# Optimization experiments

Measured on AMD Instinct MI355X. Metric: run time of the kernel, lower is better.

## Reference

```python
import jax, jax.numpy as jnp
import numpy as np

B, T, D, H = 2, 2048, 1024, 16
DK = D // H


def setup_inputs() -> dict:
    key = jax.random.key(0)
    ks = jax.random.split(key, 9)
    x = jax.random.normal(ks[0], (B, T, D), dtype=jnp.float32)
    # causal mask, broadcastable to [B, H, T, T]; positions with 0 are masked
    mask = jnp.tril(jnp.ones((T, T), dtype=jnp.int32))[None, None]
    s = 1.0 / np.sqrt(D)
    Wq = jax.random.normal(ks[1], (D, D), dtype=jnp.float32) * s
    Wk = jax.random.normal(ks[2], (D, D), dtype=jnp.float32) * s
    Wv = jax.random.normal(ks[3], (D, D), dtype=jnp.float32) * s
    Wo = jax.random.normal(ks[4], (D, D), dtype=jnp.float32) * s
    bq = jnp.zeros((D,), jnp.float32)
    bk = jnp.zeros((D,), jnp.float32)
    bv = jnp.zeros((D,), jnp.float32)
    bo = jnp.zeros((D,), jnp.float32)
    return {"x": x, "mask": mask, "Wq": Wq, "bq": bq, "Wk": Wk, "bk": bk,
            "Wv": Wv, "bv": bv, "Wo": Wo, "bo": bo}


def _split_heads(t):
    # [B, T, D] -> [B, H, T, DK]
    return t.reshape(B, T, H, DK).transpose(0, 2, 1, 3)


def reference(x, mask, Wq, bq, Wk, bk, Wv, bv, Wo, bo):
    Q = _split_heads(x @ Wq.T + bq)
    K = _split_heads(x @ Wk.T + bk)
    V = _split_heads(x @ Wv.T + bv)
    scores = jnp.einsum('bhqd,bhkd->bhqk', Q, K) / jnp.sqrt(jnp.float32(DK))
    scores = jnp.where(mask == 0, jnp.float32(-1e9), scores)
    attn = jax.nn.softmax(scores, axis=-1)  # dropout p=0 -> identity
    out = jnp.einsum('bhqk,bhkd->bhqd', attn, V)
    out = out.transpose(0, 2, 1, 3).reshape(B, T, D)
    out = out @ Wo.T + bo
    return (out, attn)
```

## Files before the change

### kernel.cpp

```cpp
#include <hip/hip_runtime.h>
#include <hip/hip_bf16.h>
#include <cstdint>


typedef __attribute__((ext_vector_type(8))) short bf16x8;
typedef __attribute__((ext_vector_type(4))) float f32x4;

#define MFMA(a,b,c) __builtin_amdgcn_mfma_f32_16x16x32_bf16((a),(b),(c),0,0,0)

static __device__ __forceinline__ short f2bf(float f) {
  __hip_bfloat16 h = __float2bfloat16(f);
  return (short)__builtin_bit_cast(ushort, h);
}

static __device__ __forceinline__ bf16x8 cvt8(const float* p) {
  float4 v0 = *(const float4*)p;
  float4 v1 = *(const float4*)(p + 4);
  bf16x8 r;
  r[0] = f2bf(v0.x); r[1] = f2bf(v0.y); r[2] = f2bf(v0.z); r[3] = f2bf(v0.w);
  r[4] = f2bf(v1.x); r[5] = f2bf(v1.y); r[6] = f2bf(v1.z); r[7] = f2bf(v1.w);
  return r;
}

static __device__ __forceinline__ size_t wbf_off(int J, int k) {
  return (size_t)((J >> 9) * 2048 + 1536 + (J & 511)) * 4096 + k;
}

__global__ __launch_bounds__(256)
void cvt_xw(const float* __restrict__ x,
            const float* __restrict__ Wq, const float* __restrict__ Wk,
            const float* __restrict__ Wv,
            ushort* __restrict__ xbf, ushort* __restrict__ attnU)
{
  if (blockIdx.x < 2048) {
    const size_t i = ((size_t)blockIdx.x * 256 + threadIdx.x) * 8;
    *(bf16x8*)&xbf[i] = cvt8(x + i);
  } else {
    const size_t e = ((size_t)(blockIdx.x - 2048) * 256 + threadIdx.x) * 8;
    const int J = (int)(e >> 10);
    const int k = (int)(e & 1023);
    const int widx = J >> 10, j = J & 1023;
    const float* W = (widx == 0) ? Wq : ((widx == 1) ? Wk : Wv);
    const bf16x8 v = cvt8(W + (size_t)j * 1024 + k);
    *(bf16x8*)&attnU[wbf_off(J, k)] = v;
  }
}

__global__ __launch_bounds__(256)
void qkv_zeros(const ushort* __restrict__ Xbf, const ushort* __restrict__ WbfU,
               const float* __restrict__ bq, const float* __restrict__ bk,
               const float* __restrict__ bv,
               ushort* __restrict__ Qw, ushort* __restrict__ Kw, ushort* __restrict__ Vt,
               float* __restrict__ attn)
{
  __shared__ __align__(16) ushort As[128 * 32];
  __shared__ __align__(16) ushort Bs[128 * 32];
  const int tid  = threadIdx.x;
  const int lane = tid & 63;
  const int wid  = tid >> 6;

  if (blockIdx.x >= 768) {
    const int zi = blockIdx.x - 768;
    const int qtile = zi % 31;
    const int bh = zi / 31;
    const int zstart = (qtile + 1) * 64;
    const int zlen = 2048 - zstart;
    float* base = attn + ((size_t)bh * 2048 + qtile * 64) * 2048;
    const f32x4 z = (f32x4){0.f, 0.f, 0.f, 0.f};
#pragma unroll
    for (int rr = 0; rr < 16; ++rr) {
      float* rowp = base + (size_t)(wid * 16 + rr) * 2048 + zstart;
      for (int c = lane * 4; c < zlen; c += 256)
        __builtin_nontemporal_store(z, (f32x4*)(rowp + c));
    }
    return;
  }

  const int wr = wid >> 1, wc = wid & 1;
  const int g = lane >> 4, c16 = lane & 15;
  const int i0 = (blockIdx.x & 31) * 128;
  const int j0 = (blockIdx.x >> 5) * 128;

  const int widx = j0 >> 10;
  const int jj0  = j0 & 1023;
  const float* bias = (widx == 0) ? bq : ((widx == 1) ? bk : bv);

  const int arow = tid >> 2;
  const int acol = (tid & 3) * 8;
  const ushort* a0p = Xbf + (size_t)(i0 + arow) * 1024 + acol;
  const ushort* a1p = a0p + (size_t)64 * 1024;
  const int J0 = widx * 1024 + jj0 + arow;
  const ushort* b0p = WbfU + wbf_off(J0, acol);
  const ushort* b1p = WbfU + wbf_off(J0 + 64, acol);

  f32x4 acc[4][4];
#pragma unroll
  for (int mi = 0; mi < 4; ++mi)
#pragma unroll
    for (int ni = 0; ni < 4; ++ni) acc[mi][ni] = (f32x4){0.f, 0.f, 0.f, 0.f};

  for (int k0 = 0; k0 < 1024; k0 += 32) {
    const bf16x8 va0 = *(const bf16x8*)(a0p + k0);
    const bf16x8 va1 = *(const bf16x8*)(a1p + k0);
    const bf16x8 vb0 = *(const bf16x8*)(b0p + k0);
    const bf16x8 vb1 = *(const bf16x8*)(b1p + k0);
    __syncthreads();
    *(bf16x8*)&As[tid * 8]        = va0;
    *(bf16x8*)&As[2048 + tid * 8] = va1;
    *(bf16x8*)&Bs[tid * 8]        = vb0;
    *(bf16x8*)&Bs[2048 + tid * 8] = vb1;
    __syncthreads();
    bf16x8 af[4], bfv[4];
#pragma unroll
    for (int mi = 0; mi < 4; ++mi)
      af[mi] = *(const bf16x8*)&As[(wr * 64 + mi * 16 + c16) * 32 + g * 8];
#pragma unroll
    for (int ni = 0; ni < 4; ++ni)
      bfv[ni] = *(const bf16x8*)&Bs[(wc * 64 + ni * 16 + c16) * 32 + g * 8];
#pragma unroll
    for (int mi = 0; mi < 4; ++mi)
#pragma unroll
      for (int ni = 0; ni < 4; ++ni)
        acc[mi][ni] = MFMA(af[mi], bfv[ni], acc[mi][ni]);
  }

  float bv4[4];
#pragma unroll
  for (int ni = 0; ni < 4; ++ni) bv4[ni] = bias[jj0 + wc * 64 + ni * 16 + c16];

  if (widx < 2) {
    ushort* OP = (widx == 0) ? Qw : Kw;
#pragma unroll
    for (int mi = 0; mi < 4; ++mi) {
      const int ib = i0 + wr * 64 + mi * 16 + g * 4;
      const int b = ib >> 11, t = ib & 2047;
#pragma unroll
      for (int ni = 0; ni < 4; ++ni) {
        const int jj = jj0 + wc * 64 + ni * 16 + c16;
        const int h = jj >> 6, dk = jj & 63;
        const size_t base = ((size_t)(b * 16 + h) * 2048 + t) * 64 + dk;
#pragma unroll
        for (int r = 0; r < 4; ++r)
          OP[base + (size_t)r * 64] = (ushort)f2bf(acc[mi][ni][r] + bv4[ni]);
      }
    }
  } else {
#pragma unroll
    for (int mi = 0; mi < 4; ++mi) {
      const int ib = i0 + wr * 64 + mi * 16 + g * 4;
      const int b = ib >> 11, t = ib & 2047;
#pragma unroll
      for (int ni = 0; ni < 4; ++ni) {
        const int jj = jj0 + wc * 64 + ni * 16 + c16;
        ushort4 pk;
        pk.x = (ushort)f2bf(acc[mi][ni][0] + bv4[ni]);
        pk.y = (ushort)f2bf(acc[mi][ni][1] + bv4[ni]);
        pk.z = (ushort)f2bf(acc[mi][ni][2] + bv4[ni]);
        pk.w = (ushort)f2bf(acc[mi][ni][3] + bv4[ni]);
        *(ushort4*)&Vt[((size_t)b * 1024 + jj) * 2048 + t] = pk;
      }
    }
  }
}

__global__ __launch_bounds__(512)
void attn_stats(const ushort* __restrict__ Qw, const ushort* __restrict__ Kw,
                const ushort* __restrict__ Vt, ushort* __restrict__ ctx,
                float* __restrict__ Linv)
{
  __shared__ __align__(16) ushort Ks[2][64][68];
  __shared__ __align__(16) ushort Vs[2][64][68];
  __shared__ __align__(16) ushort Plds[8][16][68];
  const int tid = threadIdx.x, lane = tid & 63, wid = tid >> 6;
  const int g = lane >> 4, c16 = lane & 15;
  const int pr = blockIdx.x;
  const int bh = blockIdx.y;
  const int b = bh >> 4, h = bh & 15;

  const ushort* kbase = Kw + (size_t)bh * (2048 * 64);
  const ushort* vbase = Vt + ((size_t)b * 1024 + h * 64) * 2048;

  const int sr = tid >> 3;
  const int sc = (tid & 7) * 8;
  const ushort* kst = kbase + (size_t)sr * 64 + sc;
  const ushort* vst = vbase + (size_t)sr * 2048 + sc;

  int cur = 0;

#pragma unroll
  for (int part = 0; part < 2; ++part) {
    const int jt = part ? (15 - pr) : pr;
    const int qt = jt * 128 + wid * 16;
    const int q = qt + c16;
    const int nch = 2 * jt + 2;

    const ushort* qp = Qw + ((size_t)bh * 2048 + q) * 64 + g * 8;
    const bf16x8 qf0 = *(const bf16x8*)qp;
    const bf16x8 qf1 = *(const bf16x8*)(qp + 32);

    f32x4 o[4];
#pragma unroll
    for (int dt = 0; dt < 4; ++dt) o[dt] = (f32x4){0.f, 0.f, 0.f, 0.f};
    float lsum = 0.f;

    {
      const bf16x8 k0 = *(const bf16x8*)kst;
      const bf16x8 v0 = *(const bf16x8*)vst;
      __syncthreads();
      *(bf16x8*)&Ks[cur][sr][sc] = k0;
      *(bf16x8*)&Vs[cur][sr][sc] = v0;
    }

    for (int c = 0; c < nch; ++c) {
      bf16x8 kn, vn;
      const bool pf = (c + 1 < nch);
      if (pf) {
        const int kt1 = (c + 1) * 64;
        kn = *(const bf16x8*)(kst + (size_t)kt1 * 64);
        vn = *(const bf16x8*)(vst + kt1);
      }
      __syncthreads();

      const int kt = c * 64;
      f32x4 sv[4];
#pragma unroll
      for (int s = 0; s < 4; ++s) {
        const bf16x8 kf0 = *(const bf16x8*)&Ks[cur][s * 16 + c16][g * 8];
        const bf16x8 kf1 = *(const bf16x8*)&Ks[cur][s * 16 + c16][32 + g * 8];
        f32x4 t0 = (f32x4){0.f, 0.f, 0.f, 0.f};
        t0 = MFMA(kf0, qf0, t0);
        t0 = MFMA(kf1, qf1, t0);
        sv[s] = t0;
      }

#pragma unroll
      for (int s = 0; s < 4; ++s) {
        short pk[4];
#pragma unroll
        for (int r = 0; r < 4; ++r) {
          const int k = kt + s * 16 + g * 4 + r;
          const float p = (k > q) ? 0.f : __expf(sv[s][r] * 0.125f - 20.f);
          lsum += p;
          pk[r] = f2bf(p);
        }
        *(short4*)&Plds[wid][c16][s * 16 + g * 4] = *(short4*)pk;
      }

      {
        const bf16x8 pa0 = *(const bf16x8*)&Plds[wid][c16][g * 8];
#pragma unroll
        for (int dt = 0; dt < 4; ++dt) {
          const bf16x8 vf = *(const bf16x8*)&Vs[cur][dt * 16 + c16][g * 8];
          o[dt] = MFMA(pa0, vf, o[dt]);
        }
        const bf16x8 pa1 = *(const bf16x8*)&Plds[wid][c16][32 + g * 8];
#pragma unroll
        for (int dt = 0; dt < 4; ++dt) {
          const bf16x8 vf = *(const bf16x8*)&Vs[cur][dt * 16 + c16][32 + g * 8];
          o[dt] = MFMA(pa1, vf, o[dt]);
        }
      }

      if (pf) {
        *(bf16x8*)&Ks[cur ^ 1][sr][sc] = kn;
        *(bf16x8*)&Vs[cur ^ 1][sr][sc] = vn;
        cur ^= 1;
      }
    }

    lsum += __shfl_xor(lsum, 16);
    lsum += __shfl_xor(lsum, 32);
    const float linv = 1.f / lsum;
    if (g == 0) Linv[(size_t)bh * 2048 + q] = linv;

#pragma unroll
    for (int r = 0; r < 4; ++r) {
      const float lr = __shfl(linv, g * 4 + r);
#pragma unroll
      for (int dt = 0; dt < 4; ++dt)
        ctx[((size_t)(b * 2048 + qt + g * 4 + r)) * 1024 + h * 64 + dt * 16 + c16] =
            (ushort)f2bf(o[dt][r] * lr);
    }
  }
}

__global__ __launch_bounds__(256)
void out_tiles(const ushort* __restrict__ Qw, const ushort* __restrict__ Kw,
               const float* __restrict__ Linv, float* __restrict__ attn,
               const ushort* __restrict__ ctx, const float* __restrict__ Wo,
               const float* __restrict__ bo, float* __restrict__ out)
{
  __shared__ __align__(16) ushort As[128 * 32];
  __shared__ __align__(16) ushort Bs[128 * 32];
  __shared__ __align__(16) float Pst[4][16][72];
  const int tid = threadIdx.x, lane = tid & 63, wid = tid >> 6;
  const int g = lane >> 4, c16 = lane & 15;

  if (blockIdx.x >= 256) {
    const int ti = blockIdx.x - 256;
    const int bx = ti % 132;
    const int bh = ti / 132;
    const int n = bx * 4 + wid;
    int qtile = (int)((sqrtf(8.f * n + 1.f) - 1.f) * 0.5f);
    while ((qtile + 1) * (qtile + 2) / 2 <= n) ++qtile;
    while (qtile * (qtile + 1) / 2 > n) --qtile;
    const int ktile = n - qtile * (qtile + 1) / 2;
    const int qt0 = qtile * 64, kt0 = ktile * 64;
    float* abase = attn + ((size_t)bh * 2048) * 2048;

    const ushort* qbase = Qw + ((size_t)bh * 2048 + qt0) * 64;
    const ushort* kbase = Kw + ((size_t)bh * 2048 + kt0) * 64;
    bf16x8 qf0[4], qf1[4], kf0[4], kf1[4];
    float lv[4];
#pragma unroll
    for (int sq = 0; sq < 4; ++sq) {
      const ushort* qp = qbase + (size_t)(sq * 16 + c16) * 64 + g * 8;
      qf0[sq] = *(const bf16x8*)qp;
      qf1[sq] = *(const bf16x8*)(qp + 32);
      lv[sq] = Linv[(size_t)bh * 2048 + qt0 + sq * 16 + c16];
    }
#pragma unroll
    for (int sk = 0; sk < 4; ++sk) {
      const ushort* kp = kbase + (size_t)(sk * 16 + c16) * 64 + g * 8;
      kf0[sk] = *(const bf16x8*)kp;
      kf1[sk] = *(const bf16x8*)(kp + 32);
    }

    const bool diag = (ktile == qtile);
    const int rrow = lane >> 4;
    const int rcol = (lane & 15) * 4;

#pragma unroll
    for (int sq = 0; sq < 4; ++sq) {
      const int qq = qt0 + sq * 16 + c16;
#pragma unroll
      for (int sk = 0; sk < 4; ++sk) {
        f32x4 t = (f32x4){0.f, 0.f, 0.f, 0.f};
        t = MFMA(kf0[sk], qf0[sq], t);
        t = MFMA(kf1[sk], qf1[sq], t);
        f32x4 st;
        if (diag) {
#pragma unroll
          for (int r = 0; r < 4; ++r) {
            const int kk = kt0 + sk * 16 + g * 4 + r;
            st[r] = (kk > qq) ? 0.f : __expf(t[r] * 0.125f - 20.f) * lv[sq];
          }
        } else {
#pragma unroll
          for (int r = 0; r < 4; ++r)
            st[r] = __expf(t[r] * 0.125f - 20.f) * lv[sq];
        }
        *(f32x4*)&Pst[wid][c16][sk * 16 + g * 4] = st;
      }
#pragma unroll
      for (int rr = 0; rr < 4; ++rr) {
        const int row = rr * 4 + rrow;
        const f32x4 v = *(const f32x4*)&Pst[wid][row][rcol];
        __builtin_nontemporal_store(v,
            (f32x4*)(abase + (size_t)(qt0 + sq * 16 + row) * 2048 + kt0 + rcol));
      }
    }
    return;
  }

  const int j = blockIdx.x;
  const int wr = wid >> 1, wc = wid & 1;
  const int i0 = (j & 31) * 128;
  const int j0 = (j >> 5) * 128;

  const int arow = tid >> 2;
  const int acol = (tid & 3) * 8;
  const ushort* a0p = ctx + (size_t)(i0 + arow) * 1024 + acol;
  const ushort* a1p = a0p + (size_t)64 * 1024;
  const float*  b0p = Wo + (size_t)(j0 + arow) * 1024 + acol;
  const float*  b1p = b0p + (size_t)64 * 1024;

  f32x4 acc[4][4];
#pragma unroll
  for (int mi = 0; mi < 4; ++mi)
#pragma unroll
    for (int ni = 0; ni < 4; ++ni) acc[mi][ni] = (f32x4){0.f, 0.f, 0.f, 0.f};

  for (int k0 = 0; k0 < 1024; k0 += 32) {
    const bf16x8 va0 = *(const bf16x8*)(a0p + k0);
    const bf16x8 va1 = *(const bf16x8*)(a1p + k0);
    const bf16x8 vb0 = cvt8(b0p + k0);
    const bf16x8 vb1 = cvt8(b1p + k0);
    __syncthreads();
    *(bf16x8*)&As[tid * 8]        = va0;
    *(bf16x8*)&As[2048 + tid * 8] = va1;
    *(bf16x8*)&Bs[tid * 8]        = vb0;
    *(bf16x8*)&Bs[2048 + tid * 8] = vb1;
    __syncthreads();
    bf16x8 af[4], bfv[4];
#pragma unroll
    for (int mi = 0; mi < 4; ++mi)
      af[mi] = *(const bf16x8*)&As[(wr * 64 + mi * 16 + c16) * 32 + g * 8];
#pragma unroll
    for (int ni = 0; ni < 4; ++ni)
      bfv[ni] = *(const bf16x8*)&Bs[(wc * 64 + ni * 16 + c16) * 32 + g * 8];
#pragma unroll
    for (int mi = 0; mi < 4; ++mi)
#pragma unroll
      for (int ni = 0; ni < 4; ++ni)
        acc[mi][ni] = MFMA(af[mi], bfv[ni], acc[mi][ni]);
  }

  float bv4[4];
#pragma unroll
  for (int ni = 0; ni < 4; ++ni) bv4[ni] = bo[j0 + wc * 64 + ni * 16 + c16];

#pragma unroll
  for (int mi = 0; mi < 4; ++mi) {
    const int ib = i0 + wr * 64 + mi * 16 + g * 4;
#pragma unroll
    for (int ni = 0; ni < 4; ++ni) {
      const int jj = j0 + wc * 64 + ni * 16 + c16;
#pragma unroll
      for (int r = 0; r < 4; ++r)
        out[(size_t)(ib + r) * 1024 + jj] = acc[mi][ni][r] + bv4[ni];
    }
  }
}

extern "C" void kernel_launch(void* const* d_in, const int* in_sizes, int n_in,
                              void* d_out, int out_size, void* d_ws, size_t ws_size,
                              hipStream_t stream)
{
  const float* x  = (const float*)d_in[0];
  const float* Wq = (const float*)d_in[2];
  const float* bq = (const float*)d_in[3];
  const float* Wk = (const float*)d_in[4];
  const float* bk = (const float*)d_in[5];
  const float* Wv = (const float*)d_in[6];
  const float* bv = (const float*)d_in[7];
  const float* Wo = (const float*)d_in[8];
  const float* bo = (const float*)d_in[9];

  if (ws_size < (size_t)33816576) return;

  float* out  = (float*)d_out;
  float* attn = out + (size_t)4194304;
  ushort* attnU = (ushort*)attn;

  ushort* ws   = (ushort*)d_ws;
  ushort* Qw   = ws;
  ushort* Kw   = Qw + (size_t)4194304;
  ushort* Vtw  = Kw + (size_t)4194304;
  ushort* ctx  = Vtw + (size_t)4194304;
  float*  Linv = (float*)(ctx + (size_t)4194304);

  cvt_xw<<<dim3(3584), 256, 0, stream>>>(x, Wq, Wk, Wv, ctx, attnU);
  qkv_zeros<<<dim3(1760), 256, 0, stream>>>(ctx, attnU, bq, bk, bv,
                                            Qw, Kw, Vtw, attn);
  attn_stats<<<dim3(8, 32), 512, 0, stream>>>(Qw, Kw, Vtw, ctx, Linv);
  out_tiles<<<dim3(4480), 256, 0, stream>>>(Qw, Kw, Linv, attn, ctx, Wo, bo, out);
}
```

Baseline: 220.2 us.

## Write attention probabilities as 64x256 strips staged through shared memory

The attention-probability writer now has each block cover a 64-row by 256-column strip. The four waves compute adjacent 64x64 tiles into a shared staging buffer, and the block then stores full 1 KB row segments, replacing per-wave 256-byte row pieces. Zero-filling of the masked region in the earlier kernel now starts at 256-column strip boundaries, so the strip kernel writes the zeros inside partially masked strips. This trades larger shared memory use and a block barrier for fewer, more contiguous global stores, and it reorders the strip schedule so the largest strips run first.

```diff
diff --git a/kernel.cpp b/kernel.cpp
--- a/kernel.cpp
+++ b/kernel.cpp
@@ -61,9 +61,9 @@
 
   if (blockIdx.x >= 768) {
     const int zi = blockIdx.x - 768;
-    const int qtile = zi % 31;
-    const int bh = zi / 31;
-    const int zstart = (qtile + 1) * 64;
+    const int qtile = zi % 28;
+    const int bh = zi / 28;
+    const int zstart = ((qtile >> 2) + 1) * 256;
     const int zlen = 2048 - zstart;
     float* base = attn + ((size_t)bh * 2048 + qtile * 64) * 2048;
     const f32x4 z = (f32x4){0.f, 0.f, 0.f, 0.f};
@@ -285,85 +285,96 @@
 }
 
 __global__ __launch_bounds__(256)
-void out_tiles(const ushort* __restrict__ Qw, const ushort* __restrict__ Kw,
-               const float* __restrict__ Linv, float* __restrict__ attn,
-               const ushort* __restrict__ ctx, const float* __restrict__ Wo,
-               const float* __restrict__ bo, float* __restrict__ out)
+void out_strips(const ushort* __restrict__ Qw, const ushort* __restrict__ Kw,
+                const float* __restrict__ Linv, float* __restrict__ attn,
+                const ushort* __restrict__ ctx, const float* __restrict__ Wo,
+                const float* __restrict__ bo, float* __restrict__ out)
 {
-  __shared__ __align__(16) ushort As[128 * 32];
-  __shared__ __align__(16) ushort Bs[128 * 32];
-  __shared__ __align__(16) float Pst[4][16][72];
+  __shared__ __align__(16) unsigned char smem[64 * 268 * 4];
+  ushort* As = (ushort*)smem;
+  ushort* Bs = (ushort*)(smem + 8192);
+  float*  Ps = (float*)smem;
   const int tid = threadIdx.x, lane = tid & 63, wid = tid >> 6;
   const int g = lane >> 4, c16 = lane & 15;
 
-  if (blockIdx.x >= 256) {
-    const int ti = blockIdx.x - 256;
-    const int bx = ti % 132;
-    const int bh = ti / 132;
-    const int n = bx * 4 + wid;
-    int qtile = (int)((sqrtf(8.f * n + 1.f) - 1.f) * 0.5f);
-    while ((qtile + 1) * (qtile + 2) / 2 <= n) ++qtile;
-    while (qtile * (qtile + 1) / 2 > n) --qtile;
-    const int ktile = n - qtile * (qtile + 1) / 2;
-    const int qt0 = qtile * 64, kt0 = ktile * 64;
+  if (blockIdx.x >= 8) {
+    const int s = 143 - (blockIdx.x - 8);
+    const int bh = blockIdx.y;
+    int qtile = 0, acc = 0;
+    for (;;) {
+      const int w = (qtile >> 2) + 1;
+      if (s < acc + w) break;
+      acc += w; ++qtile;
+    }
+    const int kstrip = s - acc;
+    const int qt0 = qtile * 64;
+    const int kc0 = kstrip * 256;
+    const int ktile = kstrip * 4 + wid;
     float* abase = attn + ((size_t)bh * 2048) * 2048;
 
-    const ushort* qbase = Qw + ((size_t)bh * 2048 + qt0) * 64;
-    const ushort* kbase = Kw + ((size_t)bh * 2048 + kt0) * 64;
-    bf16x8 qf0[4], qf1[4], kf0[4], kf1[4];
-    float lv[4];
-#pragma unroll
-    for (int sq = 0; sq < 4; ++sq) {
-      const ushort* qp = qbase + (size_t)(sq * 16 + c16) * 64 + g * 8;
-      qf0[sq] = *(const bf16x8*)qp;
-      qf1[sq] = *(const bf16x8*)(qp + 32);
-      lv[sq] = Linv[(size_t)bh * 2048 + qt0 + sq * 16 + c16];
-    }
-#pragma unroll
-    for (int sk = 0; sk < 4; ++sk) {
-      const ushort* kp = kbase + (size_t)(sk * 16 + c16) * 64 + g * 8;
-      kf0[sk] = *(const bf16x8*)kp;
-      kf1[sk] = *(const bf16x8*)(kp + 32);
-    }
-
-    const bool diag = (ktile == qtile);
-    const int rrow = lane >> 4;
-    const int rcol = (lane & 15) * 4;
-
-#pragma unroll
-    for (int sq = 0; sq < 4; ++sq) {
-      const int qq = qt0 + sq * 16 + c16;
+    if (ktile > qtile) {
+      const f32x4 z = (f32x4){0.f, 0.f, 0.f, 0.f};
+#pragma unroll
+      for (int sq = 0; sq < 4; ++sq)
+#pragma unroll
+        for (int sk = 0; sk < 4; ++sk)
+          *(f32x4*)&Ps[(sq * 16 + c16) * 268 + wid * 64 + sk * 16 + g * 4] = z;
+    } else {
+      const ushort* qbase = Qw + ((size_t)bh * 2048 + qt0) * 64;
+      const ushort* kbase = Kw + ((size_t)bh * 2048 + ktile * 64) * 64;
+      bf16x8 qf0[4], qf1[4], kf0[4], kf1[4];
+      float lv[4];
+#pragma unroll
+      for (int sq = 0; sq < 4; ++sq) {
+        const ushort* qp = qbase + (size_t)(sq * 16 + c16) * 64 + g * 8;
+        qf0[sq] = *(const bf16x8*)qp;
+        qf1[sq] = *(const bf16x8*)(qp + 32);
+        lv[sq] = Linv[(size_t)bh * 2048 + qt0 + sq * 16 + c16];
+      }
 #pragma unroll
       for (int sk = 0; sk < 4; ++sk) {
-        f32x4 t = (f32x4){0.f, 0.f, 0.f, 0.f};
-        t = MFMA(kf0[sk], qf0[sq], t);
-        t = MFMA(kf1[sk], qf1[sq], t);
-        f32x4 st;
-        if (diag) {
-#pragma unroll
-          for (int r = 0; r < 4; ++r) {
-            const int kk = kt0 + sk * 16 + g * 4 + r;
-            st[r] = (kk > qq) ? 0.f : __expf(t[r] * 0.125f - 20.f) * lv[sq];
+        const ushort* kp = kbase + (size_t)(sk * 16 + c16) * 64 + g * 8;
+        kf0[sk] = *(const bf16x8*)kp;
+        kf1[sk] = *(const bf16x8*)(kp + 32);
+      }
+      const bool diag = (ktile == qtile);
+#pragma unroll
+      for (int sq = 0; sq < 4; ++sq) {
+        const int qq = qt0 + sq * 16 + c16;
+#pragma unroll
+        for (int sk = 0; sk < 4; ++sk) {
+          f32x4 t = (f32x4){0.f, 0.f, 0.f, 0.f};
+          t = MFMA(kf0[sk], qf0[sq], t);
+          t = MFMA(kf1[sk], qf1[sq], t);
+          f32x4 st;
+          if (diag) {
+#pragma unroll
+            for (int r = 0; r < 4; ++r) {
+              const int kk = ktile * 64 + sk * 16 + g * 4 + r;
+              st[r] = (kk > qq) ? 0.f : __expf(t[r] * 0.125f - 20.f) * lv[sq];
+            }
+          } else {
+#pragma unroll
+            for (int r = 0; r < 4; ++r)
+              st[r] = __expf(t[r] * 0.125f - 20.f) * lv[sq];
           }
-        } else {
-#pragma unroll
-          for (int r = 0; r < 4; ++r)
-            st[r] = __expf(t[r] * 0.125f - 20.f) * lv[sq];
+          *(f32x4*)&Ps[(sq * 16 + c16) * 268 + wid * 64 + sk * 16 + g * 4] = st;
         }
-        *(f32x4*)&Pst[wid][c16][sk * 16 + g * 4] = st;
-      }
-#pragma unroll
-      for (int rr = 0; rr < 4; ++rr) {
-        const int row = rr * 4 + rrow;
-        const f32x4 v = *(const f32x4*)&Pst[wid][row][rcol];
-        __builtin_nontemporal_store(v,
-            (f32x4*)(abase + (size_t)(qt0 + sq * 16 + row) * 2048 + kt0 + rcol));
-      }
+      }
+    }
+    __syncthreads();
+    const int loff = lane * 4;
+#pragma unroll
+    for (int it = 0; it < 16; ++it) {
+      const int row = it * 4 + wid;
+      const f32x4 v = *(const f32x4*)&Ps[row * 268 + loff];
+      __builtin_nontemporal_store(v,
+          (f32x4*)(abase + (size_t)(qt0 + row) * 2048 + kc0 + loff));
     }
     return;
   }
 
-  const int j = blockIdx.x;
+  const int j = blockIdx.x * 32 + blockIdx.y;
   const int wr = wid >> 1, wc = wid & 1;
   const int i0 = (j & 31) * 128;
   const int j0 = (j >> 5) * 128;
@@ -451,8 +462,8 @@
   float*  Linv = (float*)(ctx + (size_t)4194304);
 
   cvt_xw<<<dim3(3584), 256, 0, stream>>>(x, Wq, Wk, Wv, ctx, attnU);
-  qkv_zeros<<<dim3(1760), 256, 0, stream>>>(ctx, attnU, bq, bk, bv,
+  qkv_zeros<<<dim3(1664), 256, 0, stream>>>(ctx, attnU, bq, bk, bv,
                                             Qw, Kw, Vtw, attn);
   attn_stats<<<dim3(8, 32), 512, 0, stream>>>(Qw, Kw, Vtw, ctx, Linv);
-  out_tiles<<<dim3(4480), 256, 0, stream>>>(Qw, Kw, Linv, attn, ctx, Wo, bo, out);
-}
+  out_strips<<<dim3(152, 32), 256, 0, stream>>>(Qw, Kw, Linv, attn, ctx, Wo, bo, out);
+}
```

New measurement: 233.0 us. +5.8%, slower.
